# Kernel optimization log

Hardware: AMD Instinct MI355X
Metric: run time of the kernel (lower is better)

Reference implementation:

```python
import jax, jax.numpy as jnp
import numpy as np


def setup_inputs() -> dict:
    key = jax.random.key(0)
    k1, k2, k3, k4 = jax.random.split(key, 4)
    B, N, F, H, O = 4, 2048, 256, 8, 256
    nodes = jax.random.normal(k1, (B, N, F), dtype=jnp.float32)
    W_heads = jax.random.normal(k2, (H, F, F), dtype=jnp.float32) * (1.0 / np.sqrt(F))
    W_out = jax.random.normal(k3, (H * F, O), dtype=jnp.float32) * (1.0 / np.sqrt(H * F))
    bias = jax.random.normal(k4, (O,), dtype=jnp.float32) * 0.02
    return {"nodes": nodes, "W_heads": W_heads, "W_out": W_out, "bias": bias}


def reference(nodes, W_heads, W_out, bias):
    # nodes: [B,N,F]; W_heads: [H,F,F]; W_out: [H*F,O]; bias: [O]
    B, N, F = nodes.shape
    H = W_heads.shape[0]
    norm = 1.0 / jnp.sqrt(jnp.asarray(F, dtype=nodes.dtype))
    # per-head bilinear scores: (x @ W_h) @ x^T  -> [B,H,N,N]
    xw = jnp.einsum('bnf,hfg->bhng', nodes, W_heads)
    scores = jnp.einsum('bhng,bmg->bhnm', xw, nodes) * norm
    att = jax.nn.softmax(scores, axis=-1)
    # messages: att @ x (V = input nodes) -> [B,H,N,F]
    msgs = jnp.einsum('bhnm,bmf->bhnf', att, nodes)
    # concat heads along feature axis (head 0 first) -> [B,N,H*F]
    msgs = msgs.transpose(0, 2, 1, 3).reshape(B, N, H * F)
    return jnp.matmul(msgs, W_out) + bias
```

## Files before the change

### kernel.cpp

```cpp
#include <hip/hip_runtime.h>
#include <hip/hip_bf16.h>

#define B_ 4
#define N_ 2048
#define F_ 256
#define H_ 8
#define O_ 256

#define SCALE_QK 0.09016844005556021f

typedef __attribute__((ext_vector_type(8))) short short8;
typedef __attribute__((ext_vector_type(4))) short s16x4;
typedef __attribute__((ext_vector_type(4))) float f32x4;
typedef __attribute__((ext_vector_type(4))) unsigned int u32x4;

static __device__ __forceinline__ float bf2f(short u) {
    unsigned int x = ((unsigned int)(unsigned short)u) << 16;
    return __builtin_bit_cast(float, x);
}
static __device__ __forceinline__ short f2bf(float f) {
    unsigned int x = __builtin_bit_cast(unsigned int, f);
    unsigned int lsb = (x >> 16) & 1u;
    x += 0x7fffu + lsb;
    return (short)(x >> 16);
}
static __device__ __forceinline__ unsigned int pkbf(float a, float b) {
    return (unsigned int)(unsigned short)f2bf(a) |
           ((unsigned int)(unsigned short)f2bf(b) << 16);
}

static __device__ __forceinline__ void gld16(const short* g, short* l) {
    __builtin_amdgcn_global_load_lds(
        (const __attribute__((address_space(1))) void*)g,
        (__attribute__((address_space(3))) void*)l, 16, 0, 0);
}

__global__ __launch_bounds__(256) void cvtT_kernel(const float* __restrict__ src,
                                                   short* __restrict__ dst,
                                                   int R, int C) {
    __shared__ short tile[32][33];
    src += (size_t)blockIdx.z * R * C;
    dst += (size_t)blockIdx.z * R * C;
    int tx = threadIdx.x, ty = threadIdx.y;
    int c0 = blockIdx.x * 32, r0 = blockIdx.y * 32;
#pragma unroll
    for (int j = 0; j < 4; j++) {
        int r = r0 + ty + j * 8;
        tile[ty + j * 8][tx] = f2bf(src[(size_t)r * C + c0 + tx]);
    }
    __syncthreads();
#pragma unroll
    for (int j = 0; j < 4; j++) {
        int c = c0 + ty + j * 8;
        dst[(size_t)c * R + r0 + tx] = tile[tx][ty + j * 8];
    }
}

__global__ __launch_bounds__(256) void cvt_kernel(const float* __restrict__ src,
                                                  short* __restrict__ dst, int n) {
    int i = blockIdx.x * 256 + threadIdx.x;
    if (n >= 2048) {
        size_t base = (size_t)i * 8;
#pragma unroll
        for (int j = 0; j < 8; j++) dst[base + j] = f2bf(src[base + j]);
    } else if (i < n) {
        dst[i] = f2bf(src[i]);
    }
}

template <int NCT>
__device__ __forceinline__ void gemm64_bt(const short* __restrict__ A, int lda,
                                          const short* __restrict__ Bt, int ldb,
                                          float* __restrict__ C, int ldc,
                                          int K, const short* __restrict__ bias) {
    __shared__ short sA[64][72];
    __shared__ short sB[NCT * 16][72];
    int tid = threadIdx.x;
    int w = tid >> 6, l = tid & 63, lq = l & 15, quad = l >> 4;
    f32x4 acc[NCT];
#pragma unroll
    for (int i = 0; i < NCT; i++) acc[i] = (f32x4)(0.f);

    for (int kb = 0; kb < K; kb += 64) {
        __syncthreads();
#pragma unroll
        for (int i = 0; i < 2; i++) {
            int idx = tid + i * 256; int r = idx >> 3, c = (idx & 7) * 8;
            *(short8*)&sA[r][c] = *(const short8*)&A[(size_t)r * lda + kb + c];
        }
#pragma unroll
        for (int i = 0; i < NCT / 2; i++) {
            int idx = tid + i * 256; int r = idx >> 3, c = (idx & 7) * 8;
            *(short8*)&sB[r][c] = *(const short8*)&Bt[(size_t)r * ldb + kb + c];
        }
        __syncthreads();
#pragma unroll
        for (int kk = 0; kk < 2; kk++) {
            short8 af = *(const short8*)&sA[w * 16 + lq][kk * 32 + quad * 8];
#pragma unroll
            for (int ct = 0; ct < NCT; ct++) {
                short8 bf = *(const short8*)&sB[ct * 16 + lq][kk * 32 + quad * 8];
                acc[ct] = __builtin_amdgcn_mfma_f32_16x16x32_bf16(af, bf, acc[ct], 0, 0, 0);
            }
        }
    }
#pragma unroll
    for (int ct = 0; ct < NCT; ct++) {
        int col = ct * 16 + lq;
        float bv = bias ? bf2f(bias[col]) : 0.f;
#pragma unroll
        for (int r = 0; r < 4; r++) {
            int row = w * 16 + quad * 4 + r;
            C[(size_t)row * ldc + col] = acc[ct][r] + bv;
        }
    }
}

__global__ __launch_bounds__(256) void out_kernel(const short* __restrict__ msgs,
                                                  const short* __restrict__ WoutT,
                                                  const short* __restrict__ bias,
                                                  float* __restrict__ out) {
    int mt = blockIdx.x, nt = blockIdx.y;
    gemm64_bt<4>(msgs + (size_t)mt * 64 * (H_ * F_), H_ * F_,
                 WoutT + (size_t)nt * 64 * (H_ * F_), H_ * F_,
                 out + (size_t)mt * 64 * O_ + nt * 64, O_,
                 H_ * F_, bias + nt * 64);
}


#define STAGE_KV(KT, KVF, KVTF) do {                                         \
    _Pragma("unroll")                                                        \
    for (int i_ = 0; i_ < 4; i_++) {                                         \
        int rk_ = w * 8 + i_ * 2 + (l >> 5);                                 \
        int bk_ = (l & 31) ^ (rk_ & 31);                                     \
        gld16(&Xb[(size_t)((KT) * 64 + rk_) * F_ + bk_ * 8],                 \
              &KVF[(w * 8 + i_ * 2) * 256]);                                 \
        int rt_ = w * 32 + i_ * 8 + (l >> 3);                                \
        int bt_ = (l & 7) ^ (rt_ & 7);                                       \
        gld16(&XTb[(size_t)rt_ * N_ + (KT) * 64 + bt_ * 8],                  \
              &KVTF[(w * 32 + i_ * 8) * 64]);                                \
    }                                                                        \
} while (0)

#define COMPUTE_KT(KVF, KVTF) do {                                           \
    f32x4 sacc[4];                                                           \
    _Pragma("unroll")                                                        \
    for (int ct = 0; ct < 4; ct++) sacc[ct] = (f32x4)(0.f);                  \
    _Pragma("unroll")                                                        \
    for (int kk = 0; kk < 8; kk++) {                                         \
        _Pragma("unroll")                                                    \
        for (int ct = 0; ct < 4; ct++) {                                     \
            int arow = ct * 16 + lq;                                         \
            int ab = (kk * 4 + quad) ^ (arow & 31);                          \
            short8 af = *(const short8*)&KVF[arow * 256 + ab * 8];           \
            sacc[ct] = __builtin_amdgcn_mfma_f32_16x16x32_bf16(af, aq[kk], sacc[ct], 0, 0, 0); \
        }                                                                    \
    }                                                                        \
    float mx = -INFINITY;                                                    \
    _Pragma("unroll")                                                        \
    for (int ct = 0; ct < 4; ct++)                                           \
        _Pragma("unroll")                                                    \
        for (int r_ = 0; r_ < 4; r_++) mx = fmaxf(mx, sacc[ct][r_]);         \
    mx = fmaxf(mx, __shfl_xor(mx, 16));                                      \
    mx = fmaxf(mx, __shfl_xor(mx, 32));                                      \
    float mn = fmaxf(m_q, mx);                                               \
    float alpha = exp2f(m_q - mn);                                           \
    m_q = mn;                                                                \
    float pv[4][4]; float s_ = 0.f;                                          \
    _Pragma("unroll")                                                        \
    for (int ct = 0; ct < 4; ct++)                                           \
        _Pragma("unroll")                                                    \
        for (int r_ = 0; r_ < 4; r_++) {                                     \
            pv[ct][r_] = exp2f(sacc[ct][r_] - mn);                           \
            s_ += pv[ct][r_];                                                \
        }                                                                    \
    s_ += __shfl_xor(s_, 16);                                                \
    s_ += __shfl_xor(s_, 32);                                                \
    l_q = l_q * alpha + s_;                                                  \
    if (!__all(alpha == 1.0f)) {                                             \
        _Pragma("unroll")                                                    \
        for (int ct = 0; ct < 16; ct++)                                      \
            _Pragma("unroll")                                                \
            for (int r_ = 0; r_ < 4; r_++) oacc[ct][r_] *= alpha;            \
    }                                                                        \
    unsigned int w2[4][2];                                                   \
    _Pragma("unroll")                                                        \
    for (int ct = 0; ct < 4; ct++) {                                         \
        w2[ct][0] = pkbf(pv[ct][0], pv[ct][1]);                              \
        w2[ct][1] = pkbf(pv[ct][2], pv[ct][3]);                              \
    }                                                                        \
    int sl0 = (2 * (quad & 1)) * 16 + lq;                                    \
    int sl1 = sl0 + 16;                                                      \
    bool hi = (quad >> 1) != 0;                                              \
    short8 pfrag[2];                                                         \
    _Pragma("unroll")                                                        \
    for (int kk = 0; kk < 2; kk++) {                                         \
        unsigned int u0 = __shfl((int)w2[2 * kk][0], sl0);                   \
        unsigned int u1 = __shfl((int)w2[2 * kk][1], sl0);                   \
        unsigned int u2 = __shfl((int)w2[2 * kk][0], sl1);                   \
        unsigned int u3 = __shfl((int)w2[2 * kk][1], sl1);                   \
        unsigned int v0 = __shfl((int)w2[2 * kk + 1][0], sl0);               \
        unsigned int v1 = __shfl((int)w2[2 * kk + 1][1], sl0);               \
        unsigned int v2 = __shfl((int)w2[2 * kk + 1][0], sl1);               \
        unsigned int v3 = __shfl((int)w2[2 * kk + 1][1], sl1);               \
        u32x4 pk = { hi ? v0 : u0, hi ? v1 : u1, hi ? v2 : u2, hi ? v3 : u3 }; \
        pfrag[kk] = __builtin_bit_cast(short8, pk);                          \
    }                                                                        \
    _Pragma("unroll")                                                        \
    for (int ct = 0; ct < 16; ct++) {                                        \
        int arow = ct * 16 + lq;                                             \
        short8 a0 = *(const short8*)&KVTF[arow * 64 + ((quad) ^ (arow & 7)) * 8]; \
        short8 a1 = *(const short8*)&KVTF[arow * 64 + ((4 + quad) ^ (arow & 7)) * 8]; \
        oacc[ct] = __builtin_amdgcn_mfma_f32_16x16x32_bf16(a0, pfrag[0], oacc[ct], 0, 0, 0); \
        oacc[ct] = __builtin_amdgcn_mfma_f32_16x16x32_bf16(a1, pfrag[1], oacc[ct], 0, 0, 0); \
    }                                                                        \
} while (0)

__global__ __launch_bounds__(512) void attn_kernel(const short* __restrict__ X,
                                                   const short* __restrict__ WhT,
                                                   const short* __restrict__ XT,
                                                   short* __restrict__ msgs) {
    __shared__ short kvfA[64 * 256];
    __shared__ short kvfB[64 * 256];
    __shared__ short kvTfA[256 * 64];
    __shared__ short kvTfB[256 * 64];

    int qt = blockIdx.x, bh = blockIdx.y, b = bh >> 3, h = bh & 7;
    int tid = threadIdx.x, w = tid >> 6, l = tid & 63, lq = l & 15, quad = l >> 4;
    int q0 = qt * 128;

    const short* Xb  = X  + (size_t)b * N_ * F_;
    const short* XTb = XT + (size_t)b * F_ * N_;
    const short* Whh = WhT + (size_t)h * F_ * F_;

    f32x4 oacc[16];
    short8 aq[8];

#pragma unroll
    for (int i = 0; i < 16; i++) oacc[i] = (f32x4)(0.f);
    {
        short* xdst = (w < 4) ? kvfA : kvfB;
        int wl = w & 3;
#pragma unroll
        for (int i = 0; i < 8; i++) {
            int r = wl * 16 + i * 2 + (l >> 5);
            int bb = (l & 31) ^ (r & 31);
            gld16(&Xb[(size_t)(q0 + ((w >> 2) * 64) + r) * F_ + bb * 8],
                  &xdst[(wl * 16 + i * 2) * 256]);
        }
    }
    const short* xsrc = (w < 4) ? kvfA : kvfB;
#pragma unroll 1
    for (int kb = 0; kb < 4; kb++) {
        __syncthreads();
#pragma unroll
        for (int i = 0; i < 4; i++) {
            int rt = w * 32 + i * 8 + (l >> 3);
            int bt = (l & 7) ^ (rt & 7);
            gld16(&Whh[(size_t)rt * F_ + kb * 64 + bt * 8], &kvTfA[(w * 32 + i * 8) * 64]);
        }
        __syncthreads();
#pragma unroll
        for (int kk = 0; kk < 2; kk++) {
            int arow = (w & 3) * 16 + lq;
            int ab = (kb * 8 + kk * 4 + quad) ^ (arow & 31);
            short8 af = *(const short8*)&xsrc[arow * 256 + ab * 8];
#pragma unroll
            for (int ct = 0; ct < 16; ct++) {
                int brow = ct * 16 + lq;
                int bb = (kk * 4 + quad) ^ (brow & 7);
                short8 bf = *(const short8*)&kvTfA[brow * 64 + bb * 8];
                oacc[ct] = __builtin_amdgcn_mfma_f32_16x16x32_bf16(af, bf, oacc[ct], 0, 0, 0);
            }
        }
    }
    __syncthreads();
    {
        short* qdst = (w < 4) ? kvTfA : kvTfB;
#pragma unroll
        for (int ct = 0; ct < 16; ct++) {
#pragma unroll
            for (int r = 0; r < 4; r++) {
                int row = (w & 3) * 16 + quad * 4 + r;
                int col = ct * 16 + lq;
                int pb = (col >> 3) ^ (row & 31);
                qdst[row * 256 + pb * 8 + (col & 7)] = f2bf(oacc[ct][r] * SCALE_QK);
            }
        }
        __syncthreads();
#pragma unroll
        for (int kk = 0; kk < 8; kk++) {
            int row = (w & 3) * 16 + lq;
            int ab = (kk * 4 + quad) ^ (row & 31);
            aq[kk] = *(const short8*)&qdst[row * 256 + ab * 8];
        }
    }
    __syncthreads();

#pragma unroll
    for (int i = 0; i < 16; i++) oacc[i] = (f32x4)(0.f);
    float m_q = -INFINITY, l_q = 0.f;

    STAGE_KV(0, kvfA, kvTfA);
    __syncthreads();

#pragma unroll 1
    for (int kt2 = 0; kt2 < 16; kt2++) {
        STAGE_KV(2 * kt2 + 1, kvfB, kvTfB);
        COMPUTE_KT(kvfA, kvTfA);
        __syncthreads();
        STAGE_KV((2 * kt2 + 2) & 31, kvfA, kvTfA);
        COMPUTE_KT(kvfB, kvTfB);
        __syncthreads();
    }

    float inv = 1.f / l_q;
    short* Mout = msgs + (size_t)(b * N_ + q0 + w * 16 + lq) * (H_ * F_) + h * F_;
#pragma unroll
    for (int ct = 0; ct < 16; ct++) {
        s16x4 v4 = { f2bf(oacc[ct][0] * inv), f2bf(oacc[ct][1] * inv),
                     f2bf(oacc[ct][2] * inv), f2bf(oacc[ct][3] * inv) };
        *(s16x4*)&Mout[ct * 16 + quad * 4] = v4;
    }
}

extern "C" void kernel_launch(void* const* d_in, const int* in_sizes, int n_in,
                              void* d_out, int out_size, void* d_ws, size_t ws_size,
                              hipStream_t stream) {
    const float* nodes = (const float*)d_in[0];
    const float* Wh    = (const float*)d_in[1];
    const float* Wout  = (const float*)d_in[2];
    const float* bias  = (const float*)d_in[3];
    float* out = (float*)d_out;

    char* ws = (char*)d_ws;
    short* msgs   = (short*)(ws);
    short* WhT    = (short*)(ws + 33554432);
    short* WoutT  = (short*)(ws + 34603008);
    short* XT     = (short*)(ws + 35651584);
    short* Xbf    = (short*)(ws + 39845888);
    short* biasbf = (short*)(ws + 44040192);

    dim3 tblk(32, 8, 1);
    hipLaunchKernelGGL(cvtT_kernel, dim3(8, 8, 8),  tblk, 0, stream, Wh,    WhT,   256,  256);
    hipLaunchKernelGGL(cvtT_kernel, dim3(8, 64, 1), tblk, 0, stream, Wout,  WoutT, 2048, 256);
    hipLaunchKernelGGL(cvtT_kernel, dim3(8, 64, 4), tblk, 0, stream, nodes, XT,    2048, 256);
    hipLaunchKernelGGL(cvt_kernel,  dim3(1024), dim3(256), 0, stream, nodes, Xbf, 2097152);
    hipLaunchKernelGGL(cvt_kernel,  dim3(1),    dim3(256), 0, stream, bias, biasbf, 256);

    hipLaunchKernelGGL(attn_kernel, dim3(16, 32), dim3(512), 0, stream, Xbf, WhT, XT, msgs);
    hipLaunchKernelGGL(out_kernel,  dim3(128, 4), dim3(256), 0, stream, msgs, WoutT, biasbf, out);
}
```

Measured before the change: 293.3 us.

## Halve KV tile to 32 keys and add setprio around MFMA phases

```diff
diff --git a/kernel.cpp b/kernel.cpp
--- a/kernel.cpp
+++ b/kernel.cpp
@@ -130,35 +130,37 @@
 
 #define STAGE_KV(KT, KVF, KVTF) do {                                         \
     _Pragma("unroll")                                                        \
-    for (int i_ = 0; i_ < 4; i_++) {                                         \
-        int rk_ = w * 8 + i_ * 2 + (l >> 5);                                 \
+    for (int i_ = 0; i_ < 2; i_++) {                                         \
+        int rk_ = w * 4 + i_ * 2 + (l >> 5);                                 \
         int bk_ = (l & 31) ^ (rk_ & 31);                                     \
-        gld16(&Xb[(size_t)((KT) * 64 + rk_) * F_ + bk_ * 8],                 \
-              &KVF[(w * 8 + i_ * 2) * 256]);                                 \
-        int rt_ = w * 32 + i_ * 8 + (l >> 3);                                \
-        int bt_ = (l & 7) ^ (rt_ & 7);                                       \
-        gld16(&XTb[(size_t)rt_ * N_ + (KT) * 64 + bt_ * 8],                  \
-              &KVTF[(w * 32 + i_ * 8) * 64]);                                \
+        gld16(&Xb[(size_t)((KT) * 32 + rk_) * F_ + bk_ * 8],                 \
+              &KVF[(w * 4 + i_ * 2) * 256]);                                 \
+        int rt_ = w * 32 + i_ * 16 + (l >> 2);                               \
+        int bt_ = (l & 3) ^ (rt_ & 3);                                       \
+        gld16(&XTb[(size_t)rt_ * N_ + (KT) * 32 + bt_ * 8],                  \
+              &KVTF[(w * 32 + i_ * 16) * 32]);                               \
     }                                                                        \
 } while (0)
 
 #define COMPUTE_KT(KVF, KVTF) do {                                           \
-    f32x4 sacc[4];                                                           \
-    _Pragma("unroll")                                                        \
-    for (int ct = 0; ct < 4; ct++) sacc[ct] = (f32x4)(0.f);                  \
+    f32x4 sacc[2];                                                           \
+    _Pragma("unroll")                                                        \
+    for (int ct = 0; ct < 2; ct++) sacc[ct] = (f32x4)(0.f);                  \
+    __builtin_amdgcn_s_setprio(1);                                           \
     _Pragma("unroll")                                                        \
     for (int kk = 0; kk < 8; kk++) {                                         \
         _Pragma("unroll")                                                    \
-        for (int ct = 0; ct < 4; ct++) {                                     \
+        for (int ct = 0; ct < 2; ct++) {                                     \
             int arow = ct * 16 + lq;                                         \
             int ab = (kk * 4 + quad) ^ (arow & 31);                          \
             short8 af = *(const short8*)&KVF[arow * 256 + ab * 8];           \
             sacc[ct] = __builtin_amdgcn_mfma_f32_16x16x32_bf16(af, aq[kk], sacc[ct], 0, 0, 0); \
         }                                                                    \
     }                                                                        \
+    __builtin_amdgcn_s_setprio(0);                                           \
     float mx = -INFINITY;                                                    \
     _Pragma("unroll")                                                        \
-    for (int ct = 0; ct < 4; ct++)                                           \
+    for (int ct = 0; ct < 2; ct++)                                           \
         _Pragma("unroll")                                                    \
         for (int r_ = 0; r_ < 4; r_++) mx = fmaxf(mx, sacc[ct][r_]);         \
     mx = fmaxf(mx, __shfl_xor(mx, 16));                                      \
@@ -166,9 +168,9 @@
     float mn = fmaxf(m_q, mx);                                               \
     float alpha = exp2f(m_q - mn);                                           \
     m_q = mn;                                                                \
-    float pv[4][4]; float s_ = 0.f;                                          \
-    _Pragma("unroll")                                                        \
-    for (int ct = 0; ct < 4; ct++)                                           \
+    float pv[2][4]; float s_ = 0.f;                                          \
+    _Pragma("unroll")                                                        \
+    for (int ct = 0; ct < 2; ct++)                                           \
         _Pragma("unroll")                                                    \
         for (int r_ = 0; r_ < 4; r_++) {                                     \
             pv[ct][r_] = exp2f(sacc[ct][r_] - mn);                           \
@@ -183,47 +185,47 @@
             _Pragma("unroll")                                                \
             for (int r_ = 0; r_ < 4; r_++) oacc[ct][r_] *= alpha;            \
     }                                                                        \
-    unsigned int w2[4][2];                                                   \
-    _Pragma("unroll")                                                        \
-    for (int ct = 0; ct < 4; ct++) {                                         \
+    unsigned int w2[2][2];                                                   \
+    _Pragma("unroll")                                                        \
+    for (int ct = 0; ct < 2; ct++) {                                         \
         w2[ct][0] = pkbf(pv[ct][0], pv[ct][1]);                              \
         w2[ct][1] = pkbf(pv[ct][2], pv[ct][3]);                              \
     }                                                                        \
     int sl0 = (2 * (quad & 1)) * 16 + lq;                                    \
     int sl1 = sl0 + 16;                                                      \
     bool hi = (quad >> 1) != 0;                                              \
-    short8 pfrag[2];                                                         \
-    _Pragma("unroll")                                                        \
-    for (int kk = 0; kk < 2; kk++) {                                         \
-        unsigned int u0 = __shfl((int)w2[2 * kk][0], sl0);                   \
-        unsigned int u1 = __shfl((int)w2[2 * kk][1], sl0);                   \
-        unsigned int u2 = __shfl((int)w2[2 * kk][0], sl1);                   \
-        unsigned int u3 = __shfl((int)w2[2 * kk][1], sl1);                   \
-        unsigned int v0 = __shfl((int)w2[2 * kk + 1][0], sl0);               \
-        unsigned int v1 = __shfl((int)w2[2 * kk + 1][1], sl0);               \
-        unsigned int v2 = __shfl((int)w2[2 * kk + 1][0], sl1);               \
-        unsigned int v3 = __shfl((int)w2[2 * kk + 1][1], sl1);               \
+    short8 pfrag;                                                            \
+    {                                                                        \
+        unsigned int u0 = __shfl((int)w2[0][0], sl0);                        \
+        unsigned int u1 = __shfl((int)w2[0][1], sl0);                        \
+        unsigned int u2 = __shfl((int)w2[0][0], sl1);                        \
+        unsigned int u3 = __shfl((int)w2[0][1], sl1);                        \
+        unsigned int v0 = __shfl((int)w2[1][0], sl0);                        \
+        unsigned int v1 = __shfl((int)w2[1][1], sl0);                        \
+        unsigned int v2 = __shfl((int)w2[1][0], sl1);                        \
+        unsigned int v3 = __shfl((int)w2[1][1], sl1);                        \
         u32x4 pk = { hi ? v0 : u0, hi ? v1 : u1, hi ? v2 : u2, hi ? v3 : u3 }; \
-        pfrag[kk] = __builtin_bit_cast(short8, pk);                          \
-    }                                                                        \
+        pfrag = __builtin_bit_cast(short8, pk);                              \
+    }                                                                        \
+    __builtin_amdgcn_s_setprio(1);                                           \
     _Pragma("unroll")                                                        \
     for (int ct = 0; ct < 16; ct++) {                                        \
         int arow = ct * 16 + lq;                                             \
-        short8 a0 = *(const short8*)&KVTF[arow * 64 + ((quad) ^ (arow & 7)) * 8]; \
-        short8 a1 = *(const short8*)&KVTF[arow * 64 + ((4 + quad) ^ (arow & 7)) * 8]; \
-        oacc[ct] = __builtin_amdgcn_mfma_f32_16x16x32_bf16(a0, pfrag[0], oacc[ct], 0, 0, 0); \
-        oacc[ct] = __builtin_amdgcn_mfma_f32_16x16x32_bf16(a1, pfrag[1], oacc[ct], 0, 0, 0); \
-    }                                                                        \
+        short8 a0 = *(const short8*)&KVTF[arow * 32 + (quad ^ (arow & 3)) * 8]; \
+        oacc[ct] = __builtin_amdgcn_mfma_f32_16x16x32_bf16(a0, pfrag, oacc[ct], 0, 0, 0); \
+    }                                                                        \
+    __builtin_amdgcn_s_setprio(0);                                           \
 } while (0)
 
-__global__ __launch_bounds__(512) void attn_kernel(const short* __restrict__ X,
-                                                   const short* __restrict__ WhT,
-                                                   const short* __restrict__ XT,
-                                                   short* __restrict__ msgs) {
-    __shared__ short kvfA[64 * 256];
-    __shared__ short kvfB[64 * 256];
-    __shared__ short kvTfA[256 * 64];
-    __shared__ short kvTfB[256 * 64];
+__global__ __launch_bounds__(512, 4) void attn_kernel(const short* __restrict__ X,
+                                                      const short* __restrict__ WhT,
+                                                      const short* __restrict__ XT,
+                                                      short* __restrict__ msgs) {
+    __shared__ short kvfA[8192];
+    __shared__ short kvfB[8192];
+    __shared__ short kvTfA[8192];
+    __shared__ short kvTfB[8192];
+    __shared__ short wbuf[8192];
 
     int qt = blockIdx.x, bh = blockIdx.y, b = bh >> 3, h = bh & 7;
     int tid = threadIdx.x, w = tid >> 6, l = tid & 63, lq = l & 15, quad = l >> 4;
@@ -238,61 +240,54 @@
 
 #pragma unroll
     for (int i = 0; i < 16; i++) oacc[i] = (f32x4)(0.f);
-    {
-        short* xdst = (w < 4) ? kvfA : kvfB;
-        int wl = w & 3;
-#pragma unroll
-        for (int i = 0; i < 8; i++) {
-            int r = wl * 16 + i * 2 + (l >> 5);
-            int bb = (l & 31) ^ (r & 31);
-            gld16(&Xb[(size_t)(q0 + ((w >> 2) * 64) + r) * F_ + bb * 8],
-                  &xdst[(wl * 16 + i * 2) * 256]);
-        }
-    }
-    const short* xsrc = (w < 4) ? kvfA : kvfB;
+    short* xbuf = (w < 2) ? kvfA : (w < 4) ? kvfB : (w < 6) ? kvTfA : kvTfB;
+#pragma unroll
+    for (int i_ = 0; i_ < 8; i_++) {
+        int rloc = (w & 1) * 16 + i_ * 2 + (l >> 5);
+        int bk = (l & 31) ^ (rloc & 31);
+        gld16(&Xb[(size_t)(q0 + w * 16 + i_ * 2 + (l >> 5)) * F_ + bk * 8],
+              &xbuf[((w & 1) * 16 + i_ * 2) * 256]);
+    }
 #pragma unroll 1
-    for (int kb = 0; kb < 4; kb++) {
-        __syncthreads();
-#pragma unroll
-        for (int i = 0; i < 4; i++) {
-            int rt = w * 32 + i * 8 + (l >> 3);
-            int bt = (l & 7) ^ (rt & 7);
-            gld16(&Whh[(size_t)rt * F_ + kb * 64 + bt * 8], &kvTfA[(w * 32 + i * 8) * 64]);
-        }
-        __syncthreads();
-#pragma unroll
-        for (int kk = 0; kk < 2; kk++) {
-            int arow = (w & 3) * 16 + lq;
-            int ab = (kb * 8 + kk * 4 + quad) ^ (arow & 31);
-            short8 af = *(const short8*)&xsrc[arow * 256 + ab * 8];
-#pragma unroll
-            for (int ct = 0; ct < 16; ct++) {
-                int brow = ct * 16 + lq;
-                int bb = (kk * 4 + quad) ^ (brow & 7);
-                short8 bf = *(const short8*)&kvTfA[brow * 64 + bb * 8];
-                oacc[ct] = __builtin_amdgcn_mfma_f32_16x16x32_bf16(af, bf, oacc[ct], 0, 0, 0);
-            }
+    for (int kb = 0; kb < 8; kb++) {
+        __syncthreads();
+#pragma unroll
+        for (int i_ = 0; i_ < 2; i_++) {
+            int rt_ = w * 32 + i_ * 16 + (l >> 2);
+            int bt_ = (l & 3) ^ (rt_ & 3);
+            gld16(&Whh[(size_t)rt_ * F_ + kb * 32 + bt_ * 8],
+                  &wbuf[(w * 32 + i_ * 16) * 32]);
+        }
+        __syncthreads();
+        int arow = (w & 1) * 16 + lq;
+        int ab = (kb * 4 + quad) ^ (arow & 31);
+        short8 af = *(const short8*)&xbuf[arow * 256 + ab * 8];
+#pragma unroll
+        for (int ct = 0; ct < 16; ct++) {
+            int brow = ct * 16 + lq;
+            int bb = quad ^ (brow & 3);
+            short8 bf = *(const short8*)&wbuf[brow * 32 + bb * 8];
+            oacc[ct] = __builtin_amdgcn_mfma_f32_16x16x32_bf16(af, bf, oacc[ct], 0, 0, 0);
         }
     }
     __syncthreads();
     {
-        short* qdst = (w < 4) ? kvTfA : kvTfB;
 #pragma unroll
         for (int ct = 0; ct < 16; ct++) {
 #pragma unroll
             for (int r = 0; r < 4; r++) {
-                int row = (w & 3) * 16 + quad * 4 + r;
+                int row = (w & 1) * 16 + quad * 4 + r;
                 int col = ct * 16 + lq;
                 int pb = (col >> 3) ^ (row & 31);
-                qdst[row * 256 + pb * 8 + (col & 7)] = f2bf(oacc[ct][r] * SCALE_QK);
+                xbuf[row * 256 + pb * 8 + (col & 7)] = f2bf(oacc[ct][r] * SCALE_QK);
             }
         }
         __syncthreads();
 #pragma unroll
         for (int kk = 0; kk < 8; kk++) {
-            int row = (w & 3) * 16 + lq;
+            int row = (w & 1) * 16 + lq;
             int ab = (kk * 4 + quad) ^ (row & 31);
-            aq[kk] = *(const short8*)&qdst[row * 256 + ab * 8];
+            aq[kk] = *(const short8*)&xbuf[row * 256 + ab * 8];
         }
     }
     __syncthreads();
@@ -305,11 +300,11 @@
     __syncthreads();
 
 #pragma unroll 1
-    for (int kt2 = 0; kt2 < 16; kt2++) {
+    for (int kt2 = 0; kt2 < 32; kt2++) {
         STAGE_KV(2 * kt2 + 1, kvfB, kvTfB);
         COMPUTE_KT(kvfA, kvTfA);
         __syncthreads();
-        STAGE_KV((2 * kt2 + 2) & 31, kvfA, kvTfA);
+        STAGE_KV((2 * kt2 + 2) & 63, kvfA, kvTfA);
         COMPUTE_KT(kvfB, kvTfB);
         __syncthreads();
     }
```

Measured after the change: 628.9 us. 114% more time.

## Process two heads per attention block to reuse staged K/V tiles

Applied to the files above, without the earlier changes.

```diff
diff --git a/kernel.cpp b/kernel.cpp
--- a/kernel.cpp
+++ b/kernel.cpp
@@ -143,9 +143,12 @@
 } while (0)
 
 #define COMPUTE_KT(KVF, KVTF) do {                                           \
-    f32x4 sacc[4];                                                           \
-    _Pragma("unroll")                                                        \
-    for (int ct = 0; ct < 4; ct++) sacc[ct] = (f32x4)(0.f);                  \
+    f32x4 sacc[2][4];                                                        \
+    _Pragma("unroll")                                                        \
+    for (int hh = 0; hh < 2; hh++)                                           \
+        _Pragma("unroll")                                                    \
+        for (int ct = 0; ct < 4; ct++) sacc[hh][ct] = (f32x4)(0.f);          \
+    __builtin_amdgcn_s_setprio(1);                                           \
     _Pragma("unroll")                                                        \
     for (int kk = 0; kk < 8; kk++) {                                         \
         _Pragma("unroll")                                                    \
@@ -153,91 +156,98 @@
             int arow = ct * 16 + lq;                                         \
             int ab = (kk * 4 + quad) ^ (arow & 31);                          \
             short8 af = *(const short8*)&KVF[arow * 256 + ab * 8];           \
-            sacc[ct] = __builtin_amdgcn_mfma_f32_16x16x32_bf16(af, aq[kk], sacc[ct], 0, 0, 0); \
+            sacc[0][ct] = __builtin_amdgcn_mfma_f32_16x16x32_bf16(af, aq[0][kk], sacc[0][ct], 0, 0, 0); \
+            sacc[1][ct] = __builtin_amdgcn_mfma_f32_16x16x32_bf16(af, aq[1][kk], sacc[1][ct], 0, 0, 0); \
         }                                                                    \
     }                                                                        \
-    float mx = -INFINITY;                                                    \
-    _Pragma("unroll")                                                        \
-    for (int ct = 0; ct < 4; ct++)                                           \
-        _Pragma("unroll")                                                    \
-        for (int r_ = 0; r_ < 4; r_++) mx = fmaxf(mx, sacc[ct][r_]);         \
-    mx = fmaxf(mx, __shfl_xor(mx, 16));                                      \
-    mx = fmaxf(mx, __shfl_xor(mx, 32));                                      \
-    float mn = fmaxf(m_q, mx);                                               \
-    float alpha = exp2f(m_q - mn);                                           \
-    m_q = mn;                                                                \
-    float pv[4][4]; float s_ = 0.f;                                          \
-    _Pragma("unroll")                                                        \
-    for (int ct = 0; ct < 4; ct++)                                           \
-        _Pragma("unroll")                                                    \
-        for (int r_ = 0; r_ < 4; r_++) {                                     \
-            pv[ct][r_] = exp2f(sacc[ct][r_] - mn);                           \
-            s_ += pv[ct][r_];                                                \
-        }                                                                    \
-    s_ += __shfl_xor(s_, 16);                                                \
-    s_ += __shfl_xor(s_, 32);                                                \
-    l_q = l_q * alpha + s_;                                                  \
-    if (!__all(alpha == 1.0f)) {                                             \
-        _Pragma("unroll")                                                    \
-        for (int ct = 0; ct < 16; ct++)                                      \
-            _Pragma("unroll")                                                \
-            for (int r_ = 0; r_ < 4; r_++) oacc[ct][r_] *= alpha;            \
-    }                                                                        \
-    unsigned int w2[4][2];                                                   \
-    _Pragma("unroll")                                                        \
-    for (int ct = 0; ct < 4; ct++) {                                         \
-        w2[ct][0] = pkbf(pv[ct][0], pv[ct][1]);                              \
-        w2[ct][1] = pkbf(pv[ct][2], pv[ct][3]);                              \
-    }                                                                        \
+    __builtin_amdgcn_s_setprio(0);                                           \
+    short8 pfrag[2][2];                                                      \
     int sl0 = (2 * (quad & 1)) * 16 + lq;                                    \
     int sl1 = sl0 + 16;                                                      \
     bool hi = (quad >> 1) != 0;                                              \
-    short8 pfrag[2];                                                         \
-    _Pragma("unroll")                                                        \
-    for (int kk = 0; kk < 2; kk++) {                                         \
-        unsigned int u0 = __shfl((int)w2[2 * kk][0], sl0);                   \
-        unsigned int u1 = __shfl((int)w2[2 * kk][1], sl0);                   \
-        unsigned int u2 = __shfl((int)w2[2 * kk][0], sl1);                   \
-        unsigned int u3 = __shfl((int)w2[2 * kk][1], sl1);                   \
-        unsigned int v0 = __shfl((int)w2[2 * kk + 1][0], sl0);               \
-        unsigned int v1 = __shfl((int)w2[2 * kk + 1][1], sl0);               \
-        unsigned int v2 = __shfl((int)w2[2 * kk + 1][0], sl1);               \
-        unsigned int v3 = __shfl((int)w2[2 * kk + 1][1], sl1);               \
-        u32x4 pk = { hi ? v0 : u0, hi ? v1 : u1, hi ? v2 : u2, hi ? v3 : u3 }; \
-        pfrag[kk] = __builtin_bit_cast(short8, pk);                          \
+    _Pragma("unroll")                                                        \
+    for (int hh = 0; hh < 2; hh++) {                                         \
+        float mx = -INFINITY;                                                \
+        _Pragma("unroll")                                                    \
+        for (int ct = 0; ct < 4; ct++)                                       \
+            _Pragma("unroll")                                                \
+            for (int r_ = 0; r_ < 4; r_++) mx = fmaxf(mx, sacc[hh][ct][r_]); \
+        mx = fmaxf(mx, __shfl_xor(mx, 16));                                  \
+        mx = fmaxf(mx, __shfl_xor(mx, 32));                                  \
+        float mn = fmaxf(m_q[hh], mx);                                       \
+        float alpha = exp2f(m_q[hh] - mn);                                   \
+        m_q[hh] = mn;                                                        \
+        float pv[4][4]; float s_ = 0.f;                                      \
+        _Pragma("unroll")                                                    \
+        for (int ct = 0; ct < 4; ct++)                                       \
+            _Pragma("unroll")                                                \
+            for (int r_ = 0; r_ < 4; r_++) {                                 \
+                pv[ct][r_] = exp2f(sacc[hh][ct][r_] - mn);                   \
+                s_ += pv[ct][r_];                                            \
+            }                                                                \
+        s_ += __shfl_xor(s_, 16);                                            \
+        s_ += __shfl_xor(s_, 32);                                            \
+        l_q[hh] = l_q[hh] * alpha + s_;                                      \
+        if (!__all(alpha == 1.0f)) {                                         \
+            _Pragma("unroll")                                                \
+            for (int ct = 0; ct < 16; ct++)                                  \
+                _Pragma("unroll")                                            \
+                for (int r_ = 0; r_ < 4; r_++) oacc[hh][ct][r_] *= alpha;    \
+        }                                                                    \
+        unsigned int w2[4][2];                                               \
+        _Pragma("unroll")                                                    \
+        for (int ct = 0; ct < 4; ct++) {                                     \
+            w2[ct][0] = pkbf(pv[ct][0], pv[ct][1]);                          \
+            w2[ct][1] = pkbf(pv[ct][2], pv[ct][3]);                          \
+        }                                                                    \
+        _Pragma("unroll")                                                    \
+        for (int kk = 0; kk < 2; kk++) {                                     \
+            unsigned int u0 = __shfl((int)w2[2 * kk][0], sl0);               \
+            unsigned int u1 = __shfl((int)w2[2 * kk][1], sl0);               \
+            unsigned int u2 = __shfl((int)w2[2 * kk][0], sl1);               \
+            unsigned int u3 = __shfl((int)w2[2 * kk][1], sl1);               \
+            unsigned int v0 = __shfl((int)w2[2 * kk + 1][0], sl0);           \
+            unsigned int v1 = __shfl((int)w2[2 * kk + 1][1], sl0);           \
+            unsigned int v2 = __shfl((int)w2[2 * kk + 1][0], sl1);           \
+            unsigned int v3 = __shfl((int)w2[2 * kk + 1][1], sl1);           \
+            u32x4 pk = { hi ? v0 : u0, hi ? v1 : u1, hi ? v2 : u2, hi ? v3 : u3 }; \
+            pfrag[hh][kk] = __builtin_bit_cast(short8, pk);                  \
+        }                                                                    \
     }                                                                        \
+    __builtin_amdgcn_s_setprio(1);                                           \
     _Pragma("unroll")                                                        \
     for (int ct = 0; ct < 16; ct++) {                                        \
         int arow = ct * 16 + lq;                                             \
         short8 a0 = *(const short8*)&KVTF[arow * 64 + ((quad) ^ (arow & 7)) * 8]; \
         short8 a1 = *(const short8*)&KVTF[arow * 64 + ((4 + quad) ^ (arow & 7)) * 8]; \
-        oacc[ct] = __builtin_amdgcn_mfma_f32_16x16x32_bf16(a0, pfrag[0], oacc[ct], 0, 0, 0); \
-        oacc[ct] = __builtin_amdgcn_mfma_f32_16x16x32_bf16(a1, pfrag[1], oacc[ct], 0, 0, 0); \
+        oacc[0][ct] = __builtin_amdgcn_mfma_f32_16x16x32_bf16(a0, pfrag[0][0], oacc[0][ct], 0, 0, 0); \
+        oacc[0][ct] = __builtin_amdgcn_mfma_f32_16x16x32_bf16(a1, pfrag[0][1], oacc[0][ct], 0, 0, 0); \
+        oacc[1][ct] = __builtin_amdgcn_mfma_f32_16x16x32_bf16(a0, pfrag[1][0], oacc[1][ct], 0, 0, 0); \
+        oacc[1][ct] = __builtin_amdgcn_mfma_f32_16x16x32_bf16(a1, pfrag[1][1], oacc[1][ct], 0, 0, 0); \
     }                                                                        \
+    __builtin_amdgcn_s_setprio(0);                                           \
 } while (0)
 
-__global__ __launch_bounds__(512) void attn_kernel(const short* __restrict__ X,
-                                                   const short* __restrict__ WhT,
-                                                   const short* __restrict__ XT,
-                                                   short* __restrict__ msgs) {
+__global__ __launch_bounds__(512, 2) void attn_kernel(const short* __restrict__ X,
+                                                      const short* __restrict__ WhT,
+                                                      const short* __restrict__ XT,
+                                                      short* __restrict__ msgs) {
     __shared__ short kvfA[64 * 256];
     __shared__ short kvfB[64 * 256];
     __shared__ short kvTfA[256 * 64];
     __shared__ short kvTfB[256 * 64];
 
-    int qt = blockIdx.x, bh = blockIdx.y, b = bh >> 3, h = bh & 7;
+    int qt = blockIdx.x, bh = blockIdx.y, b = bh >> 2, h0 = (bh & 3) * 2;
     int tid = threadIdx.x, w = tid >> 6, l = tid & 63, lq = l & 15, quad = l >> 4;
     int q0 = qt * 128;
 
-    const short* Xb  = X  + (size_t)b * N_ * F_;
-    const short* XTb = XT + (size_t)b * F_ * N_;
-    const short* Whh = WhT + (size_t)h * F_ * F_;
-
-    f32x4 oacc[16];
-    short8 aq[8];
-
-#pragma unroll
-    for (int i = 0; i < 16; i++) oacc[i] = (f32x4)(0.f);
+    const short* Xb   = X  + (size_t)b * N_ * F_;
+    const short* XTb  = XT + (size_t)b * F_ * N_;
+    const short* Whh0 = WhT + (size_t)h0 * F_ * F_;
+
+    f32x4 oacc[2][16];
+    short8 aq[2][8];
+
     {
         short* xdst = (w < 4) ? kvfA : kvfB;
         int wl = w & 3;
@@ -250,56 +260,64 @@
         }
     }
     const short* xsrc = (w < 4) ? kvfA : kvfB;
+#pragma unroll
+    for (int hh = 0; hh < 2; hh++) {
+#pragma unroll
+        for (int i = 0; i < 16; i++) oacc[hh][i] = (f32x4)(0.f);
 #pragma unroll 1
-    for (int kb = 0; kb < 4; kb++) {
-        __syncthreads();
-#pragma unroll
-        for (int i = 0; i < 4; i++) {
-            int rt = w * 32 + i * 8 + (l >> 3);
-            int bt = (l & 7) ^ (rt & 7);
-            gld16(&Whh[(size_t)rt * F_ + kb * 64 + bt * 8], &kvTfA[(w * 32 + i * 8) * 64]);
-        }
-        __syncthreads();
-#pragma unroll
-        for (int kk = 0; kk < 2; kk++) {
-            int arow = (w & 3) * 16 + lq;
-            int ab = (kb * 8 + kk * 4 + quad) ^ (arow & 31);
-            short8 af = *(const short8*)&xsrc[arow * 256 + ab * 8];
+        for (int kb = 0; kb < 4; kb++) {
+            __syncthreads();
+#pragma unroll
+            for (int i = 0; i < 4; i++) {
+                int rt = w * 32 + i * 8 + (l >> 3);
+                int bt = (l & 7) ^ (rt & 7);
+                gld16(&Whh0[(size_t)(hh * F_ * F_ + rt * F_) + kb * 64 + bt * 8],
+                      &kvTfA[(w * 32 + i * 8) * 64]);
+            }
+            __syncthreads();
+#pragma unroll
+            for (int kk = 0; kk < 2; kk++) {
+                int arow = (w & 3) * 16 + lq;
+                int ab = (kb * 8 + kk * 4 + quad) ^ (arow & 31);
+                short8 af = *(const short8*)&xsrc[arow * 256 + ab * 8];
+#pragma unroll
+                for (int ct = 0; ct < 16; ct++) {
+                    int brow = ct * 16 + lq;
+                    int bb = (kk * 4 + quad) ^ (brow & 7);
+                    short8 bf = *(const short8*)&kvTfA[brow * 64 + bb * 8];
+                    oacc[hh][ct] = __builtin_amdgcn_mfma_f32_16x16x32_bf16(af, bf, oacc[hh][ct], 0, 0, 0);
+                }
+            }
+        }
+        __syncthreads();
+        {
+            short* qdst = (w < 4) ? kvTfA : kvTfB;
 #pragma unroll
             for (int ct = 0; ct < 16; ct++) {
-                int brow = ct * 16 + lq;
-                int bb = (kk * 4 + quad) ^ (brow & 7);
-                short8 bf = *(const short8*)&kvTfA[brow * 64 + bb * 8];
-                oacc[ct] = __builtin_amdgcn_mfma_f32_16x16x32_bf16(af, bf, oacc[ct], 0, 0, 0);
+#pragma unroll
+                for (int r = 0; r < 4; r++) {
+                    int row = (w & 3) * 16 + quad * 4 + r;
+                    int col = ct * 16 + lq;
+                    int pb = (col >> 3) ^ (row & 31);
+                    qdst[row * 256 + pb * 8 + (col & 7)] = f2bf(oacc[hh][ct][r] * SCALE_QK);
+                }
+            }
+            __syncthreads();
+#pragma unroll
+            for (int kk = 0; kk < 8; kk++) {
+                int row = (w & 3) * 16 + lq;
+                int ab = (kk * 4 + quad) ^ (row & 31);
+                aq[hh][kk] = *(const short8*)&qdst[row * 256 + ab * 8];
             }
         }
     }
     __syncthreads();
-    {
-        short* qdst = (w < 4) ? kvTfA : kvTfB;
-#pragma unroll
-        for (int ct = 0; ct < 16; ct++) {
-#pragma unroll
-            for (int r = 0; r < 4; r++) {
-                int row = (w & 3) * 16 + quad * 4 + r;
-                int col = ct * 16 + lq;
-                int pb = (col >> 3) ^ (row & 31);
-                qdst[row * 256 + pb * 8 + (col & 7)] = f2bf(oacc[ct][r] * SCALE_QK);
-            }
-        }
-        __syncthreads();
-#pragma unroll
-        for (int kk = 0; kk < 8; kk++) {
-            int row = (w & 3) * 16 + lq;
-            int ab = (kk * 4 + quad) ^ (row & 31);
-            aq[kk] = *(const short8*)&qdst[row * 256 + ab * 8];
-        }
-    }
-    __syncthreads();
-
-#pragma unroll
-    for (int i = 0; i < 16; i++) oacc[i] = (f32x4)(0.f);
-    float m_q = -INFINITY, l_q = 0.f;
+
+#pragma unroll
+    for (int hh = 0; hh < 2; hh++)
+#pragma unroll
+        for (int i = 0; i < 16; i++) oacc[hh][i] = (f32x4)(0.f);
+    float m_q[2] = { -INFINITY, -INFINITY }, l_q[2] = { 0.f, 0.f };
 
     STAGE_KV(0, kvfA, kvTfA);
     __syncthreads();
@@ -314,13 +332,16 @@
         __syncthreads();
     }
 
-    float inv = 1.f / l_q;
-    short* Mout = msgs + (size_t)(b * N_ + q0 + w * 16 + lq) * (H_ * F_) + h * F_;
-#pragma unroll
-    for (int ct = 0; ct < 16; ct++) {
-        s16x4 v4 = { f2bf(oacc[ct][0] * inv), f2bf(oacc[ct][1] * inv),
-                     f2bf(oacc[ct][2] * inv), f2bf(oacc[ct][3] * inv) };
-        *(s16x4*)&Mout[ct * 16 + quad * 4] = v4;
+#pragma unroll
+    for (int hh = 0; hh < 2; hh++) {
+        float inv = 1.f / l_q[hh];
+        short* Mout = msgs + (size_t)(b * N_ + q0 + w * 16 + lq) * (H_ * F_) + (h0 + hh) * F_;
+#pragma unroll
+        for (int ct = 0; ct < 16; ct++) {
+            s16x4 v4 = { f2bf(oacc[hh][ct][0] * inv), f2bf(oacc[hh][ct][1] * inv),
+                         f2bf(oacc[hh][ct][2] * inv), f2bf(oacc[hh][ct][3] * inv) };
+            *(s16x4*)&Mout[ct * 16 + quad * 4] = v4;
+        }
     }
 }
 
@@ -348,6 +369,6 @@
     hipLaunchKernelGGL(cvt_kernel,  dim3(1024), dim3(256), 0, stream, nodes, Xbf, 2097152);
     hipLaunchKernelGGL(cvt_kernel,  dim3(1),    dim3(256), 0, stream, bias, biasbf, 256);
 
-    hipLaunchKernelGGL(attn_kernel, dim3(16, 32), dim3(512), 0, stream, Xbf, WhT, XT, msgs);
+    hipLaunchKernelGGL(attn_kernel, dim3(16, 16), dim3(512), 0, stream, Xbf, WhT, XT, msgs);
     hipLaunchKernelGGL(out_kernel,  dim3(128, 4), dim3(256), 0, stream, msgs, WoutT, biasbf, out);
 }
```

New measurement: 389.7 us. 1.33x slower.
